# Kernel tuning notes

Hardware: AMD Instinct MI355X
Metric: run time of the kernel (lower is better)

The kernel has to match this reference:

```python
import jax, jax.numpy as jnp
import numpy as np

B, S, D, H = 4, 2048, 1024, 16
DK = D // H


def _rope(x):
    # x: [B, H, S, DK]; lucidrains rotary_embedding_torch default:
    # theta=10000, interleaved (rotate_half on (d/2, 2) pairs), freqs repeated pairwise.
    s, d = x.shape[-2], x.shape[-1]
    inv_freq = 1.0 / (10000.0 ** (jnp.arange(0, d, 2, dtype=jnp.float32) / d))  # [d/2]
    angles = jnp.arange(s, dtype=jnp.float32)[:, None] * inv_freq[None, :]      # [S, d/2]
    ang = jnp.repeat(angles, 2, axis=-1)                                        # [S, d] interleaved
    cos, sin = jnp.cos(ang), jnp.sin(ang)
    xp = x.reshape(*x.shape[:-1], d // 2, 2)
    rot = jnp.stack((-xp[..., 1], xp[..., 0]), axis=-1).reshape(x.shape)        # rotate_half
    return x * cos + rot * sin


def setup_inputs() -> dict:
    key = jax.random.key(0)
    ks = jax.random.split(key, 8)
    scale = 1.0 / np.sqrt(D)
    return {
        "q": jax.random.normal(ks[0], (B, S, D), dtype=jnp.float32),
        "k": jax.random.normal(ks[1], (B, S, D), dtype=jnp.float32),
        "v": jax.random.normal(ks[2], (B, S, D), dtype=jnp.float32),
        "mask": jax.random.randint(ks[3], (B, S), 0, 2, dtype=jnp.int32),
        "w_q": jax.random.normal(ks[4], (D, D), dtype=jnp.float32) * scale,
        "w_k": jax.random.normal(ks[5], (D, D), dtype=jnp.float32) * scale,
        "w_v": jax.random.normal(ks[6], (D, D), dtype=jnp.float32) * scale,
        "w_o": jax.random.normal(ks[7], (D, D), dtype=jnp.float32) * scale,
    }


def reference(q, k, v, mask, w_q, w_k, w_v, w_o):
    # Linear weights stored [out, in] as in torch; y = x @ W^T (bias=False).
    def split_heads(x):
        b, s, _ = x.shape
        return x.reshape(b, s, H, DK).transpose(0, 2, 1, 3)  # [B,H,S,DK]

    query = split_heads(q @ w_q.T)
    key_ = split_heads(k @ w_k.T)
    value = split_heads(v @ w_v.T)

    query = _rope(query)
    key_ = _rope(key_)

    scores = jnp.einsum("bhqd,bhkd->bhqk", query, key_) / np.sqrt(DK)
    scores = jnp.where(mask[:, None, None, :] == 0, -10000.0, scores)
    attn = jax.nn.softmax(scores, axis=-1)  # dropout is identity at eval
    x = jnp.einsum("bhqk,bhkd->bhqd", attn, value)
    x = x.transpose(0, 2, 1, 3).reshape(q.shape[0], -1, H * DK)
    return x @ w_o.T
```

## Files before the change

### kernel.cpp

```cpp
#include <hip/hip_runtime.h>
#include <hip/hip_bf16.h>
#include <math.h>


namespace {

constexpr int Bb = 4, Ss = 2048, Dd = 1024, Hh = 16, DKk = 64;

typedef __bf16 bf16;
typedef __attribute__((ext_vector_type(8))) __bf16 bf16x8;
typedef __attribute__((ext_vector_type(4))) float f32x4;

__device__ __forceinline__ bf16x8 pack8(float4 a, float4 b) {
  bf16x8 r;
  r[0] = (__bf16)a.x; r[1] = (__bf16)a.y; r[2] = (__bf16)a.z; r[3] = (__bf16)a.w;
  r[4] = (__bf16)b.x; r[5] = (__bf16)b.y; r[6] = (__bf16)b.z; r[7] = (__bf16)b.w;
  return r;
}

__device__ __forceinline__ void gl_lds16(const bf16* g, bf16* l) {
  __builtin_amdgcn_global_load_lds((const __attribute__((address_space(1))) void*)g,
                                   (__attribute__((address_space(3))) void*)l, 16, 0, 0);
}

__global__ __launch_bounds__(256) void cvt_pair(const float* __restrict__ x, bf16* __restrict__ xd,
                                                const float* __restrict__ ws, bf16* __restrict__ wd) {
  const int bid = blockIdx.x;
  const float* s; bf16* d; size_t idx;
  if (bid < 4096) { s = x; d = xd; idx = (size_t)bid * 256 + threadIdx.x; }
  else { s = ws; d = wd; idx = (size_t)(bid - 4096) * 256 + threadIdx.x; }
  idx *= 8;
  float4 f0 = *(const float4*)(s + idx), f1 = *(const float4*)(s + idx + 4);
  *(bf16x8*)(d + idx) = pack8(f0, f1);
}

__global__ __launch_bounds__(256) void cvt_w(const float* __restrict__ ws, bf16* __restrict__ wd) {
  size_t idx = ((size_t)blockIdx.x * 256 + threadIdx.x) * 8;
  float4 f0 = *(const float4*)(ws + idx), f1 = *(const float4*)(ws + idx + 4);
  *(bf16x8*)(wd + idx) = pack8(f0, f1);
}

template <int MODE>
__global__ __launch_bounds__(256) void mha_gemm(const bf16* __restrict__ A,
                                                const bf16* __restrict__ W,
                                                void* __restrict__ dstv) {
  __shared__ __align__(16) bf16 As[128][32];
  __shared__ __align__(16) bf16 Bs[128][32];
  const int tid = threadIdx.x;
  const int bm0 = blockIdx.x * 128, bn0 = blockIdx.y * 128;
  const int w = tid >> 6, lane = tid & 63, l16 = lane & 15, quad = lane >> 4;
  const int wm = (w >> 1) * 64, wn = (w & 1) * 64;
  const int lr = lane >> 2, lc = (lane & 3) * 8;

  const bf16* Ag = A + (size_t)(bm0 + w * 32 + lr) * Dd + lc;
  const bf16* Wg = W + (size_t)(bn0 + w * 32 + lr) * Dd + lc;
  bf16* AsW = &As[w * 32][0];
  bf16* BsW = &Bs[w * 32][0];

  f32x4 acc[4][4] = {};

  for (int kt = 0; kt < Dd; kt += 32) {
    gl_lds16(Ag + kt, AsW);
    gl_lds16(Ag + kt + 16 * Dd, AsW + 16 * 32);
    gl_lds16(Wg + kt, BsW);
    gl_lds16(Wg + kt + 16 * Dd, BsW + 16 * 32);
    __syncthreads();
    bf16x8 af[4], bw[4];
#pragma unroll
    for (int i = 0; i < 4; ++i) af[i] = *(bf16x8*)&As[wm + i * 16 + l16][quad * 8];
#pragma unroll
    for (int i = 0; i < 4; ++i) bw[i] = *(bf16x8*)&Bs[wn + i * 16 + l16][quad * 8];
#pragma unroll
    for (int mt = 0; mt < 4; ++mt)
#pragma unroll
      for (int nt = 0; nt < 4; ++nt)
        acc[mt][nt] =
            __builtin_amdgcn_mfma_f32_16x16x32_bf16(af[mt], bw[nt], acc[mt][nt], 0, 0, 0);
    __syncthreads();
  }

  if constexpr (MODE == 2) {
    float* out = (float*)dstv;
#pragma unroll
    for (int mt = 0; mt < 4; ++mt)
#pragma unroll
      for (int nt = 0; nt < 4; ++nt) {
        const int gcol = bn0 + wn + nt * 16 + l16;
        const int grow0 = bm0 + wm + mt * 16 + quad * 4;
#pragma unroll
        for (int r = 0; r < 4; ++r) out[(size_t)(grow0 + r) * Dd + gcol] = acc[mt][nt][r];
      }
  } else if constexpr (MODE == 1) {
    bf16* vt = (bf16*)dstv;
#pragma unroll
    for (int mt = 0; mt < 4; ++mt)
#pragma unroll
      for (int nt = 0; nt < 4; ++nt) {
        const int gcol = bn0 + wn + nt * 16 + l16;
        const int h = gcol >> 6, dk = gcol & 63;
#pragma unroll
        for (int r = 0; r < 4; ++r) {
          const int grow = bm0 + wm + mt * 16 + quad * 4 + r;
          const int b = grow >> 11, s = grow & (Ss - 1);
          vt[((size_t)(b * Hh + h) * DKk + dk) * Ss + s] = (bf16)acc[mt][nt][r];
        }
      }
  } else {
    bf16* qp = (bf16*)dstv;
#pragma unroll
    for (int mt = 0; mt < 4; ++mt)
#pragma unroll
      for (int nt = 0; nt < 4; ++nt) {
        const int gcol = bn0 + wn + nt * 16 + l16;
        const int h = gcol >> 6, dk = gcol & 63;
        const float invf = exp2f((float)(dk >> 1) * -0.4152410118609203f);
        const float sgn = (dk & 1) ? 1.0f : -1.0f;
#pragma unroll
        for (int r = 0; r < 4; ++r) {
          const int grow = bm0 + wm + mt * 16 + quad * 4 + r;
          const int b = grow >> 11, s = grow & (Ss - 1);
          const float v = acc[mt][nt][r];
          const float ov = __shfl_xor(v, 1);
          float sn, cs;
          __sincosf((float)s * invf, &sn, &cs);
          const float rot = v * cs + sgn * ov * sn;
          qp[((size_t)(b * Hh + h) * Ss + s) * DKk + dk] = (bf16)rot;
        }
      }
  }
}

__global__ __launch_bounds__(256, 4) void mha_attn(const bf16* __restrict__ Qp,
                                                   const bf16* __restrict__ Kp,
                                                   const bf16* __restrict__ Vt,
                                                   const int* __restrict__ maskG,
                                                   bf16* __restrict__ Xo) {
  __shared__ __align__(16) bf16 Ks[2][64][64];
  __shared__ __align__(16) bf16 Vs[2][64][64];
  __shared__ __align__(16) bf16 QP[8][64][8];

  constexpr float c1 = 0.18033688011112042f;
  constexpr float c2 = -17.312340490667562f;

  const int tid = threadIdx.x;
  const int bh = blockIdx.y, b = bh >> 4, h = bh & 15;
  const int q0 = blockIdx.x * 64;
  const int w = tid >> 6, lane = tid & 63, l16 = lane & 15, quad = lane >> 4;
  const int swz = l16 & 7;
  const size_t hbase = (size_t)bh * Ss * DKk;

  {
    const int row = tid >> 2, seg = tid & 3;
    const bf16* src = Qp + hbase + (size_t)(q0 + row) * DKk + seg * 16;
    *(int4*)&QP[seg * 2 + 0][row][0] = *(const int4*)(src);
    *(int4*)&QP[seg * 2 + 1][row][0] = *(const int4*)(src + 8);
  }
  __syncthreads();
  bf16x8 qf[2];
#pragma unroll
  for (int kk = 0; kk < 2; ++kk)
    qf[kk] = *(bf16x8*)&QP[kk * 4 + quad][w * 16 + l16][0];

  const int srow = lane >> 3, schunk = (lane & 7) ^ (srow & 7);
  const bf16* Kg = Kp + hbase + (size_t)(w * 16 + srow) * DKk + schunk * 8;
  const bf16* Vg = Vt + ((size_t)bh * DKk + w * 16 + srow) * Ss + schunk * 8;
  const int* Mg = maskG + b * Ss + l16;

  int mcur[4], mnext[4];
#pragma unroll
  for (int i = 0; i < 2; ++i) {
    gl_lds16(Kg + (size_t)i * 8 * DKk, &Ks[0][w * 16 + i * 8][0]);
    gl_lds16(Vg + i * 8 * Ss, &Vs[0][w * 16 + i * 8][0]);
  }
#pragma unroll
  for (int nt = 0; nt < 4; ++nt) mcur[nt] = Mg[nt * 16];
  __syncthreads();

  f32x4 o[4] = {};
  f32x4 l_ = {};
  bf16* Pb = &QP[0][0][0] + w * 1024;

  for (int kt = 0; kt < 32; ++kt) {
    const int cur = kt & 1, nxt = cur ^ 1;
    if (kt < 31) {
      const size_t k0n = (size_t)(kt + 1) * 64;
#pragma unroll
      for (int i = 0; i < 2; ++i) {
        gl_lds16(Kg + k0n * DKk + (size_t)i * 8 * DKk, &Ks[nxt][w * 16 + i * 8][0]);
        gl_lds16(Vg + k0n + i * 8 * Ss, &Vs[nxt][w * 16 + i * 8][0]);
      }
#pragma unroll
      for (int nt = 0; nt < 4; ++nt) mnext[nt] = Mg[k0n + nt * 16];
    }

    f32x4 sc[4] = {};
#pragma unroll
    for (int kk = 0; kk < 2; ++kk)
#pragma unroll
      for (int nt = 0; nt < 4; ++nt) {
        bf16x8 kf = *(bf16x8*)&Ks[cur][nt * 16 + l16][((kk * 4 + quad) ^ swz) * 8];
        sc[nt] = __builtin_amdgcn_mfma_f32_16x16x32_bf16(qf[kk], kf, sc[nt], 0, 0, 0);
      }

#pragma unroll
    for (int nt = 0; nt < 4; ++nt)
#pragma unroll
      for (int r = 0; r < 4; ++r) {
        const float p = (mcur[nt] != 0) ? exp2f(fmaf(sc[nt][r], c1, c2)) : 0.0f;
        sc[nt][r] = p;
        l_[r] += p;
      }

#pragma unroll
    for (int nt = 0; nt < 4; ++nt) {
      const int c = nt * 2 + (l16 >> 3);
      const int jj = l16 & 7;
#pragma unroll
      for (int r = 0; r < 4; ++r)
        Pb[(c * 16 + quad * 4 + r) * 8 + jj] = (bf16)sc[nt][r];
    }
#pragma unroll
    for (int kk = 0; kk < 2; ++kk) {
      bf16x8 pf = *(bf16x8*)(Pb + ((kk * 4 + quad) * 16 + l16) * 8);
#pragma unroll
      for (int nt = 0; nt < 4; ++nt) {
        bf16x8 vf = *(bf16x8*)&Vs[cur][nt * 16 + l16][((kk * 4 + quad) ^ swz) * 8];
        o[nt] = __builtin_amdgcn_mfma_f32_16x16x32_bf16(pf, vf, o[nt], 0, 0, 0);
      }
    }
    __syncthreads();
#pragma unroll
    for (int nt = 0; nt < 4; ++nt) mcur[nt] = mnext[nt];
  }

#pragma unroll
  for (int d = 1; d < 16; d <<= 1)
#pragma unroll
    for (int r = 0; r < 4; ++r) l_[r] += __shfl_xor(l_[r], d);

#pragma unroll
  for (int nt = 0; nt < 4; ++nt)
#pragma unroll
    for (int r = 0; r < 4; ++r) {
      const int srw = q0 + w * 16 + quad * 4 + r;
      const int dk = nt * 16 + l16;
      Xo[(size_t)(b * Ss + srw) * Dd + h * DKk + dk] = (bf16)(o[nt][r] / l_[r]);
    }
}

}

extern "C" void kernel_launch(void* const* d_in, const int* in_sizes, int n_in,
                              void* d_out, int out_size, void* d_ws, size_t ws_size,
                              hipStream_t stream) {
  (void)in_sizes; (void)n_in; (void)out_size; (void)ws_size;
  const float* q = (const float*)d_in[0];
  const float* k = (const float*)d_in[1];
  const float* v = (const float*)d_in[2];
  const int* mask = (const int*)d_in[3];
  const float* w_q = (const float*)d_in[4];
  const float* w_k = (const float*)d_in[5];
  const float* w_v = (const float*)d_in[6];
  const float* w_o = (const float*)d_in[7];
  float* out = (float*)d_out;

  const size_t n_elem = (size_t)Bb * Hh * Ss * DKk;
  bf16* buf0 = (bf16*)d_ws;
  bf16* wbuf = buf0 + n_elem;
  bf16* Qp = wbuf + (1 << 20);
  bf16* Kp = Qp + n_elem;
  bf16* Vt = Kp + n_elem;

  dim3 g(64, 8), blk(256);
  cvt_pair<<<4608, blk, 0, stream>>>(q, buf0, w_q, wbuf);
  mha_gemm<0><<<g, blk, 0, stream>>>(buf0, wbuf, (void*)Qp);
  cvt_pair<<<4608, blk, 0, stream>>>(k, buf0, w_k, wbuf);
  mha_gemm<0><<<g, blk, 0, stream>>>(buf0, wbuf, (void*)Kp);
  cvt_pair<<<4608, blk, 0, stream>>>(v, buf0, w_v, wbuf);
  mha_gemm<1><<<g, blk, 0, stream>>>(buf0, wbuf, (void*)Vt);
  mha_attn<<<dim3(32, 64), blk, 0, stream>>>(Qp, Kp, Vt, mask, buf0);
  cvt_w<<<512, blk, 0, stream>>>(w_o, wbuf);
  mha_gemm<2><<<g, blk, 0, stream>>>(buf0, wbuf, (void*)out);
}
```

Before: 413.6 us.

## Double-buffer GEMM LDS tiles and widen attention query tile with MFMA row sums

The projection GEMM now double-buffers its A/W LDS tiles, prefetching the next K slice while the current one is multiplied. The attention kernel processes 128 queries per block, two 16-row tiles per wave, so each K/V tile loaded into LDS is reused twice and the grid is halved. The mask is folded into the score accumulator init as a -1e9 bias, and row sums are computed with an MFMA against a ones vector instead of per-element adds and shuffles. This raises register pressure and halves the number of attention blocks, which may reduce occupancy.

```diff
diff --git a/kernel.cpp b/kernel.cpp
--- a/kernel.cpp
+++ b/kernel.cpp
@@ -44,8 +44,8 @@
 __global__ __launch_bounds__(256) void mha_gemm(const bf16* __restrict__ A,
                                                 const bf16* __restrict__ W,
                                                 void* __restrict__ dstv) {
-  __shared__ __align__(16) bf16 As[128][32];
-  __shared__ __align__(16) bf16 Bs[128][32];
+  __shared__ __align__(16) bf16 As[2][128][32];
+  __shared__ __align__(16) bf16 Bs[2][128][32];
   const int tid = threadIdx.x;
   const int bm0 = blockIdx.x * 128, bn0 = blockIdx.y * 128;
   const int w = tid >> 6, lane = tid & 63, l16 = lane & 15, quad = lane >> 4;
@@ -54,22 +54,29 @@
 
   const bf16* Ag = A + (size_t)(bm0 + w * 32 + lr) * Dd + lc;
   const bf16* Wg = W + (size_t)(bn0 + w * 32 + lr) * Dd + lc;
-  bf16* AsW = &As[w * 32][0];
-  bf16* BsW = &Bs[w * 32][0];
 
   f32x4 acc[4][4] = {};
 
-  for (int kt = 0; kt < Dd; kt += 32) {
-    gl_lds16(Ag + kt, AsW);
-    gl_lds16(Ag + kt + 16 * Dd, AsW + 16 * 32);
-    gl_lds16(Wg + kt, BsW);
-    gl_lds16(Wg + kt + 16 * Dd, BsW + 16 * 32);
-    __syncthreads();
+  gl_lds16(Ag, &As[0][w * 32][0]);
+  gl_lds16(Ag + 16 * Dd, &As[0][w * 32 + 16][0]);
+  gl_lds16(Wg, &Bs[0][w * 32][0]);
+  gl_lds16(Wg + 16 * Dd, &Bs[0][w * 32 + 16][0]);
+  __syncthreads();
+
+  for (int kt = 0; kt < 32; ++kt) {
+    const int cur = kt & 1, nxt = cur ^ 1;
+    if (kt < 31) {
+      const int ko = (kt + 1) * 32;
+      gl_lds16(Ag + ko, &As[nxt][w * 32][0]);
+      gl_lds16(Ag + ko + 16 * Dd, &As[nxt][w * 32 + 16][0]);
+      gl_lds16(Wg + ko, &Bs[nxt][w * 32][0]);
+      gl_lds16(Wg + ko + 16 * Dd, &Bs[nxt][w * 32 + 16][0]);
+    }
     bf16x8 af[4], bw[4];
 #pragma unroll
-    for (int i = 0; i < 4; ++i) af[i] = *(bf16x8*)&As[wm + i * 16 + l16][quad * 8];
-#pragma unroll
-    for (int i = 0; i < 4; ++i) bw[i] = *(bf16x8*)&Bs[wn + i * 16 + l16][quad * 8];
+    for (int i = 0; i < 4; ++i) af[i] = *(bf16x8*)&As[cur][wm + i * 16 + l16][quad * 8];
+#pragma unroll
+    for (int i = 0; i < 4; ++i) bw[i] = *(bf16x8*)&Bs[cur][wn + i * 16 + l16][quad * 8];
 #pragma unroll
     for (int mt = 0; mt < 4; ++mt)
 #pragma unroll
@@ -137,29 +144,37 @@
                                                    bf16* __restrict__ Xo) {
   __shared__ __align__(16) bf16 Ks[2][64][64];
   __shared__ __align__(16) bf16 Vs[2][64][64];
-  __shared__ __align__(16) bf16 QP[8][64][8];
+  __shared__ __align__(16) bf16 Pbuf[4][1024];
 
   constexpr float c1 = 0.18033688011112042f;
   constexpr float c2 = -17.312340490667562f;
 
   const int tid = threadIdx.x;
   const int bh = blockIdx.y, b = bh >> 4, h = bh & 15;
-  const int q0 = blockIdx.x * 64;
+  const int q0 = blockIdx.x * 128;
   const int w = tid >> 6, lane = tid & 63, l16 = lane & 15, quad = lane >> 4;
   const int swz = l16 & 7;
   const size_t hbase = (size_t)bh * Ss * DKk;
 
   {
-    const int row = tid >> 2, seg = tid & 3;
-    const bf16* src = Qp + hbase + (size_t)(q0 + row) * DKk + seg * 16;
-    *(int4*)&QP[seg * 2 + 0][row][0] = *(const int4*)(src);
-    *(int4*)&QP[seg * 2 + 1][row][0] = *(const int4*)(src + 8);
+    bf16* Qst = &Ks[0][0][0];
+    const int row = tid >> 1, hf = tid & 1;
+    const bf16* src = Qp + hbase + (size_t)(q0 + row) * DKk + hf * 32;
+#pragma unroll
+    for (int cc = 0; cc < 4; ++cc)
+      *(int4*)&Qst[(((hf * 4 + cc) * 128) + row) * 8] = *(const int4*)(src + cc * 8);
   }
   __syncthreads();
-  bf16x8 qf[2];
-#pragma unroll
-  for (int kk = 0; kk < 2; ++kk)
-    qf[kk] = *(bf16x8*)&QP[kk * 4 + quad][w * 16 + l16][0];
+  bf16x8 qf[2][2];
+  {
+    const bf16* Qst = &Ks[0][0][0];
+#pragma unroll
+    for (int mt = 0; mt < 2; ++mt)
+#pragma unroll
+      for (int kk = 0; kk < 2; ++kk)
+        qf[mt][kk] = *(bf16x8*)&Qst[(((kk * 4 + quad) * 128) + w * 32 + mt * 16 + l16) * 8];
+  }
+  __syncthreads();
 
   const int srow = lane >> 3, schunk = (lane & 7) ^ (srow & 7);
   const bf16* Kg = Kp + hbase + (size_t)(w * 16 + srow) * DKk + schunk * 8;
@@ -176,9 +191,13 @@
   for (int nt = 0; nt < 4; ++nt) mcur[nt] = Mg[nt * 16];
   __syncthreads();
 
-  f32x4 o[4] = {};
-  f32x4 l_ = {};
-  bf16* Pb = &QP[0][0][0] + w * 1024;
+  f32x4 o[2][4] = {};
+  f32x4 lo[2] = {};
+  bf16* Pb = &Pbuf[w][0];
+
+  bf16x8 vones;
+#pragma unroll
+  for (int i = 0; i < 8; ++i) vones[i] = (__bf16)1.0f;
 
   for (int kt = 0; kt < 32; ++kt) {
     const int cur = kt & 1, nxt = cur ^ 1;
@@ -193,39 +212,45 @@
       for (int nt = 0; nt < 4; ++nt) mnext[nt] = Mg[k0n + nt * 16];
     }
 
-    f32x4 sc[4] = {};
-#pragma unroll
-    for (int kk = 0; kk < 2; ++kk)
-#pragma unroll
-      for (int nt = 0; nt < 4; ++nt) {
-        bf16x8 kf = *(bf16x8*)&Ks[cur][nt * 16 + l16][((kk * 4 + quad) ^ swz) * 8];
-        sc[nt] = __builtin_amdgcn_mfma_f32_16x16x32_bf16(qf[kk], kf, sc[nt], 0, 0, 0);
-      }
-
-#pragma unroll
-    for (int nt = 0; nt < 4; ++nt)
-#pragma unroll
-      for (int r = 0; r < 4; ++r) {
-        const float p = (mcur[nt] != 0) ? exp2f(fmaf(sc[nt][r], c1, c2)) : 0.0f;
-        sc[nt][r] = p;
-        l_[r] += p;
-      }
-
-#pragma unroll
-    for (int nt = 0; nt < 4; ++nt) {
-      const int c = nt * 2 + (l16 >> 3);
-      const int jj = l16 & 7;
-#pragma unroll
-      for (int r = 0; r < 4; ++r)
-        Pb[(c * 16 + quad * 4 + r) * 8 + jj] = (bf16)sc[nt][r];
-    }
-#pragma unroll
-    for (int kk = 0; kk < 2; ++kk) {
-      bf16x8 pf = *(bf16x8*)(Pb + ((kk * 4 + quad) * 16 + l16) * 8);
-#pragma unroll
-      for (int nt = 0; nt < 4; ++nt) {
-        bf16x8 vf = *(bf16x8*)&Vs[cur][nt * 16 + l16][((kk * 4 + quad) ^ swz) * 8];
-        o[nt] = __builtin_amdgcn_mfma_f32_16x16x32_bf16(pf, vf, o[nt], 0, 0, 0);
+#pragma unroll
+    for (int mt = 0; mt < 2; ++mt) {
+      f32x4 sc[4];
+#pragma unroll
+      for (int nt = 0; nt < 4; ++nt) {
+        const float bv = (mcur[nt] != 0) ? 0.0f : -1e9f;
+#pragma unroll
+        for (int r = 0; r < 4; ++r) sc[nt][r] = bv;
+      }
+#pragma unroll
+      for (int kk = 0; kk < 2; ++kk)
+#pragma unroll
+        for (int nt = 0; nt < 4; ++nt) {
+          bf16x8 kf = *(bf16x8*)&Ks[cur][nt * 16 + l16][((kk * 4 + quad) ^ swz) * 8];
+          sc[nt] = __builtin_amdgcn_mfma_f32_16x16x32_bf16(qf[mt][kk], kf, sc[nt], 0, 0, 0);
+        }
+
+#pragma unroll
+      for (int nt = 0; nt < 4; ++nt)
+#pragma unroll
+        for (int r = 0; r < 4; ++r) sc[nt][r] = exp2f(fmaf(sc[nt][r], c1, c2));
+
+#pragma unroll
+      for (int nt = 0; nt < 4; ++nt) {
+        const int c = nt * 2 + (l16 >> 3);
+        const int jj = l16 & 7;
+#pragma unroll
+        for (int r = 0; r < 4; ++r)
+          Pb[(c * 16 + quad * 4 + r) * 8 + jj] = (bf16)sc[nt][r];
+      }
+#pragma unroll
+      for (int kk = 0; kk < 2; ++kk) {
+        bf16x8 pf = *(bf16x8*)(Pb + ((kk * 4 + quad) * 16 + l16) * 8);
+        lo[mt] = __builtin_amdgcn_mfma_f32_16x16x32_bf16(pf, vones, lo[mt], 0, 0, 0);
+#pragma unroll
+        for (int nt = 0; nt < 4; ++nt) {
+          bf16x8 vf = *(bf16x8*)&Vs[cur][nt * 16 + l16][((kk * 4 + quad) ^ swz) * 8];
+          o[mt][nt] = __builtin_amdgcn_mfma_f32_16x16x32_bf16(pf, vf, o[mt][nt], 0, 0, 0);
+        }
       }
     }
     __syncthreads();
@@ -234,18 +259,15 @@
   }
 
 #pragma unroll
-  for (int d = 1; d < 16; d <<= 1)
-#pragma unroll
-    for (int r = 0; r < 4; ++r) l_[r] += __shfl_xor(l_[r], d);
-
-#pragma unroll
-  for (int nt = 0; nt < 4; ++nt)
-#pragma unroll
-    for (int r = 0; r < 4; ++r) {
-      const int srw = q0 + w * 16 + quad * 4 + r;
-      const int dk = nt * 16 + l16;
-      Xo[(size_t)(b * Ss + srw) * Dd + h * DKk + dk] = (bf16)(o[nt][r] / l_[r]);
-    }
+  for (int mt = 0; mt < 2; ++mt)
+#pragma unroll
+    for (int nt = 0; nt < 4; ++nt)
+#pragma unroll
+      for (int r = 0; r < 4; ++r) {
+        const int srw = q0 + w * 32 + mt * 16 + quad * 4 + r;
+        const int dk = nt * 16 + l16;
+        Xo[(size_t)(b * Ss + srw) * Dd + h * DKk + dk] = (bf16)(o[mt][nt][r] / lo[mt][r]);
+      }
 }
 
 }
@@ -278,7 +300,7 @@
   mha_gemm<0><<<g, blk, 0, stream>>>(buf0, wbuf, (void*)Kp);
   cvt_pair<<<4608, blk, 0, stream>>>(v, buf0, w_v, wbuf);
   mha_gemm<1><<<g, blk, 0, stream>>>(buf0, wbuf, (void*)Vt);
-  mha_attn<<<dim3(32, 64), blk, 0, stream>>>(Qp, Kp, Vt, mask, buf0);
+  mha_attn<<<dim3(16, 64), blk, 0, stream>>>(Qp, Kp, Vt, mask, buf0);
   cvt_w<<<512, blk, 0, stream>>>(w_o, wbuf);
   mha_gemm<2><<<g, blk, 0, stream>>>(buf0, wbuf, (void*)out);
 }
```

New measurement: 407.2 us. Within noise of the previous version (-1.5%).
